# Performance work log

Hardware: AMD Instinct MI355X
Metric: run time of the kernel (lower is better)

Reference implementation:

```python
import jax, jax.numpy as jnp
import numpy as np

DIM = 128
DIM1 = 128
D_MODEL = DIM + DIM1          # 256
D_INNER = 2 * D_MODEL         # expand=2 -> 512
D_STATE = 16
D_CONV = 4
DT_RANK = (D_MODEL + 15) // 16  # ceil(d_model/16) = 16
B, H, W = 4, 64, 64


def layer_norm(x, g, b, eps=1e-5):
    mu = jnp.mean(x, axis=-1, keepdims=True)
    var = jnp.mean((x - mu) ** 2, axis=-1, keepdims=True)
    return (x - mu) * jax.lax.rsqrt(var + eps) * g + b


def setup_inputs() -> dict:
    key = jax.random.key(0)
    ks = jax.random.split(key, 16)
    s = lambda k, shape, scale: (jax.random.normal(k, shape, jnp.float32) * scale)
    inp = {
        "input": jax.random.normal(ks[0], (B, DIM, H, W), jnp.float32),
        "input2": jax.random.normal(ks[1], (B, DIM1, H, W), jnp.float32),
        # MambaB params
        "ln0_g": jnp.ones((D_MODEL,), jnp.float32),
        "ln0_b": jnp.zeros((D_MODEL,), jnp.float32),
        "outp_w": s(ks[2], (D_MODEL, DIM), 1.0 / np.sqrt(D_MODEL)),
        "outp_b": jnp.zeros((DIM,), jnp.float32),
        # Mamba params
        "in_proj_w": s(ks[3], (D_MODEL, 2 * D_INNER), 1.0 / np.sqrt(D_MODEL)),
        "conv_w": s(ks[4], (D_INNER, D_CONV), 1.0 / np.sqrt(D_CONV)),
        "conv_b": jnp.zeros((D_INNER,), jnp.float32),
        "x_proj_w": s(ks[5], (D_INNER, DT_RANK + 2 * D_STATE), 1.0 / np.sqrt(D_INNER)),
        "dt_proj_w": s(ks[6], (DT_RANK, D_INNER), 1.0 / np.sqrt(DT_RANK)),
        "dt_proj_b": s(ks[7], (D_INNER,), 0.1),
        "A_log": jnp.log(jnp.tile(jnp.arange(1.0, D_STATE + 1.0, dtype=jnp.float32), (D_INNER, 1))),
        "D_param": jnp.ones((D_INNER,), jnp.float32),
        "mamba_out_w": s(ks[8], (D_INNER, D_MODEL), 1.0 / np.sqrt(D_INNER)),
    }
    return inp


def mamba(x, in_proj_w, conv_w, conv_b, x_proj_w, dt_proj_w, dt_proj_b, A_log, D_param, mamba_out_w):
    b, L, _ = x.shape
    xz = x @ in_proj_w                       # [b, L, 2*di]
    xs, z = jnp.split(xz, 2, axis=-1)
    # causal depthwise conv over sequence
    xt = xs.transpose(0, 2, 1)               # [b, di, L]
    conv = jax.lax.conv_general_dilated(
        xt, conv_w[:, None, :], window_strides=(1,),
        padding=[(D_CONV - 1, 0)], feature_group_count=D_INNER)
    xs = jax.nn.silu(conv + conv_b[None, :, None]).transpose(0, 2, 1)  # [b, L, di]
    x_dbl = xs @ x_proj_w                    # [b, L, dt_rank + 2*n]
    dt = x_dbl[..., :DT_RANK]
    Bm = x_dbl[..., DT_RANK:DT_RANK + D_STATE]
    Cm = x_dbl[..., DT_RANK + D_STATE:]
    delta = jax.nn.softplus(dt @ dt_proj_w + dt_proj_b)  # [b, L, di]
    A = -jnp.exp(A_log)                      # [di, n]

    def step(h, t):
        d_t, B_t, C_t, x_t = t               # [b,di],[b,n],[b,n],[b,di]
        dA = jnp.exp(d_t[:, :, None] * A)    # [b, di, n]
        h = h * dA + (d_t * x_t)[:, :, None] * B_t[:, None, :]
        y = jnp.einsum('bdn,bn->bd', h, C_t)
        return h, y

    h0 = jnp.zeros((b, D_INNER, D_STATE), x.dtype)
    _, ys = jax.lax.scan(step, h0, (delta.transpose(1, 0, 2), Bm.transpose(1, 0, 2),
                                    Cm.transpose(1, 0, 2), xs.transpose(1, 0, 2)))
    y = ys.transpose(1, 0, 2) + xs * D_param
    y = y * jax.nn.silu(z)
    return y @ mamba_out_w                   # [b, L, d_model]


def reference(input, input2, ln0_g, ln0_b, outp_w, outp_b, in_proj_w, conv_w, conv_b,
              x_proj_w, dt_proj_w, dt_proj_b, A_log, D_param, mamba_out_w):
    b, c, h, w = input.shape
    x = jnp.concatenate((input, input2), axis=1)            # [b, d_model, h, w]
    x = x.reshape(b, D_MODEL, h * w).transpose(0, 2, 1)     # [b, hw, d_model]
    x = layer_norm(x, ln0_g, ln0_b)
    out = mamba(x, in_proj_w, conv_w, conv_b, x_proj_w, dt_proj_w, dt_proj_b,
                A_log, D_param, mamba_out_w)
    out = out @ outp_w + outp_b                             # [b, hw, dim]
    return out.transpose(0, 2, 1).reshape(b, c, h, w)
```

## Files before the change

kernel.cpp:

```cpp
#include <hip/hip_runtime.h>
#include <hip/hip_bf16.h>
#include <math.h>

#define LSEQ 4096
#define NR   16384
#define NB   4
#define CHUNK 32
#define NCH  128

typedef short bf16x8 __attribute__((ext_vector_type(8)));
typedef float f32x4  __attribute__((ext_vector_type(4)));
typedef float f32x2  __attribute__((ext_vector_type(2)));

typedef __attribute__((address_space(1))) const void gvoid_t;
typedef __attribute__((address_space(3))) void svoid_t;

__device__ __forceinline__ void gld_lds16(void* lds, const void* g) {
    __builtin_amdgcn_global_load_lds((gvoid_t*)g, (svoid_t*)lds, 16, 0, 0);
}

__device__ __forceinline__ unsigned short to_bf16(float f) {
    union { float f; unsigned u; } x; x.f = f;
    unsigned r = (x.u + 0x7fff + ((x.u >> 16) & 1)) >> 16;
    return (unsigned short)r;
}
__device__ __forceinline__ float bf2f(unsigned short u) {
    union { unsigned u; float f; } x; x.u = ((unsigned)u) << 16;
    return x.f;
}
__device__ __forceinline__ float softplus_f(float x) {
    return x > 20.f ? x : __logf(1.f + __expf(x));
}
__device__ __forceinline__ float silu_f(float x) {
    return x / (1.f + __expf(-x));
}

__device__ __forceinline__ void pow_chain16_pk(float r, f32x2* a2) {
    float r2 = r * r;
    float r4 = r2 * r2;
    float r8 = r4 * r4;
    f32x2 v01 = { r, r2 };
    a2[0] = v01;
    a2[1] = v01 * r2;
    a2[2] = v01 * r4;
    a2[3] = a2[1] * r4;
    a2[4] = v01 * r8;
    a2[5] = a2[1] * r8;
    a2[6] = a2[2] * r8;
    a2[7] = a2[3] * r8;
}

__device__ __forceinline__ bool pow_ok16(const float* An) {
    bool ok = true;
    #pragma unroll
    for (int n = 1; n < 16; ++n) {
        float ref = (float)(n + 1) * An[0];
        ok = ok && (fabsf(An[n] - ref) <= 1e-4f * fabsf(An[n]) + 1e-30f);
    }
    return ok;
}

__global__ __launch_bounds__(256) void front_kernel(const float* __restrict__ in1,
                                                    const float* __restrict__ in2,
                                                    const float* __restrict__ g,
                                                    const float* __restrict__ beta,
                                                    const float* __restrict__ Wm,
                                                    const float* __restrict__ Wo,
                                                    const float* __restrict__ Wxp,
                                                    const float* __restrict__ A_log,
                                                    const float* __restrict__ W,
                                                    unsigned short* __restrict__ Abf,
                                                    unsigned short* __restrict__ WcT,
                                                    unsigned short* __restrict__ Wxpt,
                                                    float* __restrict__ anegp,
                                                    unsigned short* __restrict__ Wt) {
    __shared__ float tile[256][33];
    int blk = blockIdx.x;
    int tid = threadIdx.x;
    if (blk < 512) {
        __shared__ float s1[8][32], s2[8][32];
        __shared__ float smu[32], srs[32];
        int b  = blk >> 7;
        int t0 = (blk & 127) * 32;
        #pragma unroll
        for (int p = 0; p < 8; ++p) {
            int c = p * 32 + (tid >> 3);
            int toff = (tid & 7) * 4;
            const float* src = (c < 128) ? &in1[((size_t)(b * 128 + c)) * LSEQ + t0 + toff]
                                         : &in2[((size_t)(b * 128 + (c - 128))) * LSEQ + t0 + toff];
            float4 v = *(const float4*)src;
            tile[c][toff] = v.x; tile[c][toff+1] = v.y;
            tile[c][toff+2] = v.z; tile[c][toff+3] = v.w;
        }
        __syncthreads();
        {
            int t = tid & 31, gg = tid >> 5;
            float a1 = 0.f, a2 = 0.f;
            #pragma unroll
            for (int i = 0; i < 32; ++i) {
                float v = tile[gg * 32 + i][t];
                a1 += v; a2 += v * v;
            }
            s1[gg][t] = a1; s2[gg][t] = a2;
        }
        __syncthreads();
        if (tid < 32) {
            float a1 = 0.f, a2 = 0.f;
            #pragma unroll
            for (int gg = 0; gg < 8; ++gg) { a1 += s1[gg][tid]; a2 += s2[gg][tid]; }
            float m = a1 * (1.f / 256.f);
            float var = a2 * (1.f / 256.f) - m * m;
            smu[tid] = m;
            srs[tid] = rsqrtf(var + 1e-5f);
        }
        __syncthreads();
        int c = tid;
        float gc = g[c], bc = beta[c];
        #pragma unroll 4
        for (int t = 0; t < 32; ++t) {
            float v = (tile[c][t] - smu[t]) * srs[t] * gc + bc;
            Abf[((size_t)((b << 12) + t0 + t)) * 256 + c] = to_bf16(v);
        }
    } else if (blk < 768) {
        int gid = (blk - 512) * 256 + tid;
        int row = gid >> 7, col = gid & 127;
        float acc = 0.f;
        #pragma unroll 8
        for (int k = 0; k < 256; ++k) acc += Wm[row * 256 + k] * Wo[k * 128 + col];
        WcT[(size_t)col * 512 + row] = to_bf16(acc);
    } else if (blk < 864) {
        int gid = (blk - 768) * 256 + tid;
        int n = gid >> 9, k = gid & 511;
        Wxpt[gid] = to_bf16(Wxp[(size_t)k * 48 + n]);
    } else if (blk < 896) {
        int gid = (blk - 864) * 256 + tid;
        anegp[gid] = -__expf(A_log[gid]);
    } else {
        float* tf = &tile[0][0];
        int local = blk - 896;
        int k0 = (local & 3) * 64;
        int n0 = (local >> 2) * 64;
        int a = tid & 63, q = tid >> 6;
        #pragma unroll
        for (int i = 0; i < 16; ++i) {
            int k = q * 16 + i;
            tf[k * 65 + a] = W[(size_t)(k0 + k) * 1024 + n0 + a];
        }
        __syncthreads();
        #pragma unroll
        for (int i = 0; i < 16; ++i) {
            int n = q * 16 + i;
            Wt[(size_t)(n0 + n) * 256 + k0 + a] = to_bf16(tf[a * 65 + n]);
        }
    }
}

__global__ __launch_bounds__(256) void gemm1_mfma(const unsigned short* __restrict__ Abf,
                                                  const unsigned short* __restrict__ Wt,
                                                  unsigned short* __restrict__ xh,
                                                  unsigned short* __restrict__ zs) {
    __shared__ __align__(16) short Asl[128][32];
    __shared__ __align__(16) short Bsl[128][32];
    int tid = threadIdx.x;
    int wv = tid >> 6, ln = tid & 63;
    int m0 = blockIdx.x * 128;
    int n0 = blockIdx.y * 128;
    int mw = (wv & 1) * 64, nw = (wv >> 1) * 64;

    f32x4 acc[4][4];
    #pragma unroll
    for (int i = 0; i < 4; ++i)
        #pragma unroll
        for (int j = 0; j < 4; ++j) acc[i][j] = (f32x4)(0.f);

    int srow  = ln >> 2;
    int skoff = (ln & 3) * 8;

    for (int k0 = 0; k0 < 256; k0 += 32) {
        #pragma unroll
        for (int i = 0; i < 2; ++i) {
            int j = wv * 2 + i;
            int row = j * 16 + srow;
            gld_lds16(&Asl[j * 16][0], &Abf[(size_t)(m0 + row) * 256 + k0 + skoff]);
            gld_lds16(&Bsl[j * 16][0], &Wt [(size_t)(n0 + row) * 256 + k0 + skoff]);
        }
        __syncthreads();
        bf16x8 af[4], bff[4];
        int fm = ln & 15, fk = (ln >> 4) * 8;
        #pragma unroll
        for (int i = 0; i < 4; ++i) {
            af[i]  = *(const bf16x8*)&Asl[mw + i * 16 + fm][fk];
            bff[i] = *(const bf16x8*)&Bsl[nw + i * 16 + fm][fk];
        }
        #pragma unroll
        for (int i = 0; i < 4; ++i)
            #pragma unroll
            for (int j = 0; j < 4; ++j)
                acc[i][j] = __builtin_amdgcn_mfma_f32_16x16x32_bf16(af[i], bff[j], acc[i][j], 0, 0, 0);
        __syncthreads();
    }
    int ccol = ln & 15, crow = (ln >> 4) * 4;
    bool zhalf = (n0 >= 512);
    #pragma unroll
    for (int i = 0; i < 4; ++i) {
        #pragma unroll
        for (int j = 0; j < 4; ++j) {
            int n = n0 + nw + j * 16 + ccol;
            #pragma unroll
            for (int r = 0; r < 4; ++r) {
                int m = m0 + mw + i * 16 + crow + r;
                float v = acc[i][j][r];
                if (zhalf) zs[(size_t)m * 512 + (n - 512)] = to_bf16(silu_f(v));
                else       xh[(size_t)m * 512 + n]         = to_bf16(v);
            }
        }
    }
}

__global__ __launch_bounds__(512, 4) void mid_kernel(const unsigned short* __restrict__ xh,
                                                     const float* __restrict__ cw,
                                                     const float* __restrict__ cb,
                                                     const unsigned short* __restrict__ Wxpt,
                                                     const float* __restrict__ Wdt,
                                                     const float* __restrict__ dtb,
                                                     const float* __restrict__ anegp,
                                                     unsigned* __restrict__ dxp,
                                                     float* __restrict__ xdbl,
                                                     float* __restrict__ Sarr,
                                                     float* __restrict__ Harr) {
    __shared__ __align__(16) unsigned short xcs[CHUNK][520];
    __shared__ __align__(16) float xds[CHUNK][48];
    int tid = threadIdx.x;
    int chunk = blockIdx.x & (NCH - 1);
    int b     = blockIdx.x >> 7;
    int d = tid;
    int rbase = (b << 12) + chunk * CHUNK;

    float4 w4 = *(const float4*)&cw[d * 4];
    float cbd = cb[d];
    float An[16];
    #pragma unroll
    for (int n = 0; n < 16; n += 4) {
        float4 v = *(const float4*)&anegp[d * 16 + n];
        An[n] = v.x; An[n+1] = v.y; An[n+2] = v.z; An[n+3] = v.w;
    }
    f32x2 wdt2[8];
    #pragma unroll
    for (int q = 0; q < 8; ++q) {
        wdt2[q].x = Wdt[(2 * q) * 512 + d];
        wdt2[q].y = Wdt[(2 * q + 1) * 512 + d];
    }
    float bd = dtb[d];

    float x0 = 0.f, x1 = 0.f, x2 = 0.f;
    if (chunk > 0) {
        x0 = bf2f(xh[(size_t)(rbase - 3) * 512 + d]);
        x1 = bf2f(xh[(size_t)(rbase - 2) * 512 + d]);
        x2 = bf2f(xh[(size_t)(rbase - 1) * 512 + d]);
    }
    #pragma unroll
    for (int t = 0; t < CHUNK; ++t) {
        float x3 = bf2f(xh[(size_t)(rbase + t) * 512 + d]);
        float a = x0 * w4.x + x1 * w4.y + x2 * w4.z + x3 * w4.w + cbd;
        xcs[t][d] = to_bf16(silu_f(a));
        x0 = x1; x1 = x2; x2 = x3;
    }
    __syncthreads();

    {
        int wv = tid >> 6, ln = tid & 63;
        if (wv < 6) {
            int mt = (wv >= 3) ? 16 : 0;
            int wr = (wv >= 3) ? wv - 3 : wv;
            int nt = wr * 16;
            int fm = ln & 15, fk = (ln >> 4) * 8;
            f32x4 acc = (f32x4)(0.f);
            #pragma unroll 4
            for (int k0 = 0; k0 < 512; k0 += 32) {
                bf16x8 af  = *(const bf16x8*)&xcs[mt + fm][k0 + fk];
                bf16x8 bf_ = *(const bf16x8*)&Wxpt[(size_t)(nt + fm) * 512 + k0 + fk];
                acc = __builtin_amdgcn_mfma_f32_16x16x32_bf16(af, bf_, acc, 0, 0, 0);
            }
            int ccol = ln & 15, crow = (ln >> 4) * 4;
            #pragma unroll
            for (int r = 0; r < 4; ++r)
                xds[mt + crow + r][nt + ccol] = acc[r];
        }
    }
    __syncthreads();

    #pragma unroll
    for (int i = 0; i < 2; ++i) {
        int idx = tid + i * 512;
        int t = idx >> 5, n = idx & 31;
        xdbl[(size_t)(rbase + t) * 32 + n] = xds[t][16 + n];
    }

    bool pm = pow_ok16(An);
    f32x2 h2[8];
    #pragma unroll
    for (int n = 0; n < 8; ++n) h2[n] = (f32x2)(0.f);
    float S = 0.f;
    const float4* xds4 = (const float4*)&xds[0][0];
    if (pm) {
        float An0 = An[0];
        #pragma unroll 4
        for (int t = 0; t < CHUNK; ++t) {
            float4 q0 = xds4[t * 12 + 0], q1 = xds4[t * 12 + 1];
            float4 q2 = xds4[t * 12 + 2], q3 = xds4[t * 12 + 3];
            f32x2 acc2 = { bd, 0.f };
            acc2 = acc2 + (f32x2){q0.x, q0.y} * wdt2[0];
            acc2 = acc2 + (f32x2){q0.z, q0.w} * wdt2[1];
            acc2 = acc2 + (f32x2){q1.x, q1.y} * wdt2[2];
            acc2 = acc2 + (f32x2){q1.z, q1.w} * wdt2[3];
            acc2 = acc2 + (f32x2){q2.x, q2.y} * wdt2[4];
            acc2 = acc2 + (f32x2){q2.z, q2.w} * wdt2[5];
            acc2 = acc2 + (f32x2){q3.x, q3.y} * wdt2[6];
            acc2 = acc2 + (f32x2){q3.z, q3.w} * wdt2[7];
            float a = acc2.x + acc2.y;
            unsigned short dbf = to_bf16(softplus_f(a));
            unsigned short xbf = xcs[t][d];
            float dv = bf2f(dbf), xv = bf2f(xbf);
            dxp[(size_t)(rbase + t) * 512 + d] = (unsigned)dbf | ((unsigned)xbf << 16);
            float dx = dv * xv;
            S += dv;
            f32x2 a2[8];
            pow_chain16_pk(__expf(dv * An0), a2);
            float4 B0 = xds4[t * 12 + 4], B1 = xds4[t * 12 + 5];
            float4 B2 = xds4[t * 12 + 6], B3 = xds4[t * 12 + 7];
            h2[0] = h2[0] * a2[0] + dx * (f32x2){B0.x, B0.y};
            h2[1] = h2[1] * a2[1] + dx * (f32x2){B0.z, B0.w};
            h2[2] = h2[2] * a2[2] + dx * (f32x2){B1.x, B1.y};
            h2[3] = h2[3] * a2[3] + dx * (f32x2){B1.z, B1.w};
            h2[4] = h2[4] * a2[4] + dx * (f32x2){B2.x, B2.y};
            h2[5] = h2[5] * a2[5] + dx * (f32x2){B2.z, B2.w};
            h2[6] = h2[6] * a2[6] + dx * (f32x2){B3.x, B3.y};
            h2[7] = h2[7] * a2[7] + dx * (f32x2){B3.z, B3.w};
        }
    } else {
        #pragma unroll 2
        for (int t = 0; t < CHUNK; ++t) {
            float4 q0 = xds4[t * 12 + 0], q1 = xds4[t * 12 + 1];
            float4 q2 = xds4[t * 12 + 2], q3 = xds4[t * 12 + 3];
            f32x2 acc2 = { bd, 0.f };
            acc2 = acc2 + (f32x2){q0.x, q0.y} * wdt2[0];
            acc2 = acc2 + (f32x2){q0.z, q0.w} * wdt2[1];
            acc2 = acc2 + (f32x2){q1.x, q1.y} * wdt2[2];
            acc2 = acc2 + (f32x2){q1.z, q1.w} * wdt2[3];
            acc2 = acc2 + (f32x2){q2.x, q2.y} * wdt2[4];
            acc2 = acc2 + (f32x2){q2.z, q2.w} * wdt2[5];
            acc2 = acc2 + (f32x2){q3.x, q3.y} * wdt2[6];
            acc2 = acc2 + (f32x2){q3.z, q3.w} * wdt2[7];
            float a = acc2.x + acc2.y;
            unsigned short dbf = to_bf16(softplus_f(a));
            unsigned short xbf = xcs[t][d];
            float dv = bf2f(dbf), xv = bf2f(xbf);
            dxp[(size_t)(rbase + t) * 512 + d] = (unsigned)dbf | ((unsigned)xbf << 16);
            float dx = dv * xv;
            S += dv;
            float4 B0 = xds4[t * 12 + 4], B1 = xds4[t * 12 + 5];
            float4 B2 = xds4[t * 12 + 6], B3 = xds4[t * 12 + 7];
            f32x2 e0 = { __expf(dv * An[0]),  __expf(dv * An[1])  };
            f32x2 e1 = { __expf(dv * An[2]),  __expf(dv * An[3])  };
            f32x2 e2 = { __expf(dv * An[4]),  __expf(dv * An[5])  };
            f32x2 e3 = { __expf(dv * An[6]),  __expf(dv * An[7])  };
            f32x2 e4 = { __expf(dv * An[8]),  __expf(dv * An[9])  };
            f32x2 e5 = { __expf(dv * An[10]), __expf(dv * An[11]) };
            f32x2 e6 = { __expf(dv * An[12]), __expf(dv * An[13]) };
            f32x2 e7 = { __expf(dv * An[14]), __expf(dv * An[15]) };
            h2[0] = h2[0] * e0 + dx * (f32x2){B0.x, B0.y};
            h2[1] = h2[1] * e1 + dx * (f32x2){B0.z, B0.w};
            h2[2] = h2[2] * e2 + dx * (f32x2){B1.x, B1.y};
            h2[3] = h2[3] * e3 + dx * (f32x2){B1.z, B1.w};
            h2[4] = h2[4] * e4 + dx * (f32x2){B2.x, B2.y};
            h2[5] = h2[5] * e5 + dx * (f32x2){B2.z, B2.w};
            h2[6] = h2[6] * e6 + dx * (f32x2){B3.x, B3.y};
            h2[7] = h2[7] * e7 + dx * (f32x2){B3.z, B3.w};
        }
    }
    Sarr[(size_t)chunk * 2048 + b * 512 + d] = S;
    size_t gbase = ((size_t)(b * 512 + d)) * 16;
    size_t coff  = (size_t)chunk * 32768;
    #pragma unroll
    for (int n = 0; n < 4; ++n) {
        *(float4*)&Harr[coff + gbase + n * 4] =
            make_float4(h2[2*n].x, h2[2*n].y, h2[2*n+1].x, h2[2*n+1].y);
    }
}

__global__ __launch_bounds__(128) void scan_pass2(const float* __restrict__ Sarr,
                                                  const float* __restrict__ anegp,
                                                  float* __restrict__ Harr) {
    int gid = blockIdx.x * 128 + threadIdx.x;
    float An = anegp[gid & 8191];
    int sidx = gid >> 4;
    float carry = 0.f;
    #pragma unroll 8
    for (int c = 0; c < NCH; ++c) {
        float S  = Sarr[(size_t)c * 2048 + sidx];
        size_t off = (size_t)c * 32768 + gid;
        float he = Harr[off];
        Harr[off] = carry;
        carry = he + __expf(S * An) * carry;
    }
}

__global__ __launch_bounds__(512, 4) void scan_pass3_out(const unsigned* __restrict__ dxp,
                                                         const unsigned short* __restrict__ zs,
                                                         const float* __restrict__ xdbl,
                                                         const float* __restrict__ anegp,
                                                         const float* __restrict__ Dp,
                                                         const float* __restrict__ Hin,
                                                         const unsigned short* __restrict__ WcT,
                                                         const float* __restrict__ bo,
                                                         float* __restrict__ out) {
    __shared__ __align__(16) unsigned short yl[CHUNK][520];
    __shared__ __align__(16) float4 sB4[CHUNK][4];
    __shared__ __align__(16) float4 sC4[CHUNK][4];
    int tid = threadIdx.x;
    int chunk = blockIdx.x & (NCH - 1);
    int b     = blockIdx.x >> 7;
    int d = tid;
    int rbase = (b << 12) + chunk * CHUNK;
    unsigned pwv[CHUNK];
    #pragma unroll
    for (int t = 0; t < CHUNK; ++t)
        pwv[t] = dxp[(size_t)(rbase + t) * 512 + d];
    {
        float* sBf = (float*)sB4;
        float* sCf = (float*)sC4;
        int t = tid >> 4, n = tid & 15;
        sBf[t * 16 + n] = xdbl[(size_t)(rbase + t) * 32 + n];
        sCf[t * 16 + n] = xdbl[(size_t)(rbase + t) * 32 + 16 + n];
    }
    float An[16];
    #pragma unroll
    for (int n = 0; n < 16; n += 4) {
        float4 v = *(const float4*)&anegp[d * 16 + n];
        An[n] = v.x; An[n+1] = v.y; An[n+2] = v.z; An[n+3] = v.w;
    }
    bool pm = pow_ok16(An);
    float Dv = Dp[d];
    __syncthreads();
    size_t gbase = ((size_t)(b * 512 + d)) * 16;
    size_t coff  = (size_t)chunk * 32768;
    f32x2 h2[8];
    #pragma unroll
    for (int n = 0; n < 4; ++n) {
        float4 v = *(const float4*)&Hin[coff + gbase + n * 4];
        h2[2*n].x = v.x; h2[2*n].y = v.y; h2[2*n+1].x = v.z; h2[2*n+1].y = v.w;
    }
    if (pm) {
        float An0 = An[0];
        #pragma unroll 8
        for (int t = 0; t < CHUNK; ++t) {
            unsigned pw = pwv[t];
            float dv = bf2f((unsigned short)(pw & 0xffffu));
            float xv = bf2f((unsigned short)(pw >> 16));
            float zv = bf2f(zs[(size_t)(rbase + t) * 512 + d]);
            float dx = dv * xv;
            f32x2 a2[8];
            pow_chain16_pk(__expf(dv * An0), a2);
            float4 B0 = sB4[t][0], B1 = sB4[t][1], B2 = sB4[t][2], B3 = sB4[t][3];
            float4 C0 = sC4[t][0], C1 = sC4[t][1], C2 = sC4[t][2], C3 = sC4[t][3];
            f32x2 y2 = (f32x2)(0.f);
            h2[0] = h2[0] * a2[0] + dx * (f32x2){B0.x, B0.y};  y2 = y2 + h2[0] * (f32x2){C0.x, C0.y};
            h2[1] = h2[1] * a2[1] + dx * (f32x2){B0.z, B0.w};  y2 = y2 + h2[1] * (f32x2){C0.z, C0.w};
            h2[2] = h2[2] * a2[2] + dx * (f32x2){B1.x, B1.y};  y2 = y2 + h2[2] * (f32x2){C1.x, C1.y};
            h2[3] = h2[3] * a2[3] + dx * (f32x2){B1.z, B1.w};  y2 = y2 + h2[3] * (f32x2){C1.z, C1.w};
            h2[4] = h2[4] * a2[4] + dx * (f32x2){B2.x, B2.y};  y2 = y2 + h2[4] * (f32x2){C2.x, C2.y};
            h2[5] = h2[5] * a2[5] + dx * (f32x2){B2.z, B2.w};  y2 = y2 + h2[5] * (f32x2){C2.z, C2.w};
            h2[6] = h2[6] * a2[6] + dx * (f32x2){B3.x, B3.y};  y2 = y2 + h2[6] * (f32x2){C3.x, C3.y};
            h2[7] = h2[7] * a2[7] + dx * (f32x2){B3.z, B3.w};  y2 = y2 + h2[7] * (f32x2){C3.z, C3.w};
            float y = y2.x + y2.y + xv * Dv;
            y *= zv;
            yl[t][d] = to_bf16(y);
        }
    } else {
        #pragma unroll 4
        for (int t = 0; t < CHUNK; ++t) {
            unsigned pw = pwv[t];
            float dv = bf2f((unsigned short)(pw & 0xffffu));
            float xv = bf2f((unsigned short)(pw >> 16));
            float zv = bf2f(zs[(size_t)(rbase + t) * 512 + d]);
            float dx = dv * xv;
            float4 B0 = sB4[t][0], B1 = sB4[t][1], B2 = sB4[t][2], B3 = sB4[t][3];
            float4 C0 = sC4[t][0], C1 = sC4[t][1], C2 = sC4[t][2], C3 = sC4[t][3];
            f32x2 e0 = { __expf(dv * An[0]),  __expf(dv * An[1])  };
            f32x2 e1 = { __expf(dv * An[2]),  __expf(dv * An[3])  };
            f32x2 e2 = { __expf(dv * An[4]),  __expf(dv * An[5])  };
            f32x2 e3 = { __expf(dv * An[6]),  __expf(dv * An[7])  };
            f32x2 e4 = { __expf(dv * An[8]),  __expf(dv * An[9])  };
            f32x2 e5 = { __expf(dv * An[10]), __expf(dv * An[11]) };
            f32x2 e6 = { __expf(dv * An[12]), __expf(dv * An[13]) };
            f32x2 e7 = { __expf(dv * An[14]), __expf(dv * An[15]) };
            f32x2 y2 = (f32x2)(0.f);
            h2[0] = h2[0] * e0 + dx * (f32x2){B0.x, B0.y};  y2 = y2 + h2[0] * (f32x2){C0.x, C0.y};
            h2[1] = h2[1] * e1 + dx * (f32x2){B0.z, B0.w};  y2 = y2 + h2[1] * (f32x2){C0.z, C0.w};
            h2[2] = h2[2] * e2 + dx * (f32x2){B1.x, B1.y};  y2 = y2 + h2[2] * (f32x2){C1.x, C1.y};
            h2[3] = h2[3] * e3 + dx * (f32x2){B1.z, B1.w};  y2 = y2 + h2[3] * (f32x2){C1.z, C1.w};
            h2[4] = h2[4] * e4 + dx * (f32x2){B2.x, B2.y};  y2 = y2 + h2[4] * (f32x2){C2.x, C2.y};
            h2[5] = h2[5] * e5 + dx * (f32x2){B2.z, B2.w};  y2 = y2 + h2[5] * (f32x2){C2.z, C2.w};
            h2[6] = h2[6] * e6 + dx * (f32x2){B3.x, B3.y};  y2 = y2 + h2[6] * (f32x2){C3.x, C3.y};
            h2[7] = h2[7] * e7 + dx * (f32x2){B3.z, B3.w};  y2 = y2 + h2[7] * (f32x2){C3.z, C3.w};
            float y = y2.x + y2.y + xv * Dv;
            y *= zv;
            yl[t][d] = to_bf16(y);
        }
    }
    __syncthreads();

    {
        int wv = tid >> 6, ln = tid & 63;
        int fm = ln & 15, fk = (ln >> 4) * 8;
        f32x4 acc0 = (f32x4)(0.f), acc1 = (f32x4)(0.f);
        const unsigned short* wrow = &WcT[(size_t)(wv * 16 + fm) * 512];
        #pragma unroll 4
        for (int k0 = 0; k0 < 512; k0 += 32) {
            bf16x8 af = *(const bf16x8*)&wrow[k0 + fk];
            bf16x8 b0 = *(const bf16x8*)&yl[fm][k0 + fk];
            bf16x8 b1 = *(const bf16x8*)&yl[16 + fm][k0 + fk];
            acc0 = __builtin_amdgcn_mfma_f32_16x16x32_bf16(af, b0, acc0, 0, 0, 0);
            acc1 = __builtin_amdgcn_mfma_f32_16x16x32_bf16(af, b1, acc1, 0, 0, 0);
        }
        int ccol = ln & 15, crow = (ln >> 4) * 4;
        #pragma unroll
        for (int r = 0; r < 4; ++r) {
            int c = wv * 16 + crow + r;
            float bias = bo[c];
            size_t obase = ((size_t)(b * 128 + c)) * LSEQ + chunk * CHUNK;
            out[obase + ccol]      = acc0[r] + bias;
            out[obase + 16 + ccol] = acc1[r] + bias;
        }
    }
}

extern "C" void kernel_launch(void* const* d_in, const int* in_sizes, int n_in,
                              void* d_out, int out_size, void* d_ws, size_t ws_size,
                              hipStream_t stream) {
    (void)in_sizes; (void)n_in; (void)out_size; (void)ws_size;
    const float* input    = (const float*)d_in[0];
    const float* input2   = (const float*)d_in[1];
    const float* ln_g     = (const float*)d_in[2];
    const float* ln_b     = (const float*)d_in[3];
    const float* outp_w   = (const float*)d_in[4];
    const float* outp_b   = (const float*)d_in[5];
    const float* in_proj  = (const float*)d_in[6];
    const float* conv_w   = (const float*)d_in[7];
    const float* conv_b   = (const float*)d_in[8];
    const float* x_proj   = (const float*)d_in[9];
    const float* dt_w     = (const float*)d_in[10];
    const float* dt_b     = (const float*)d_in[11];
    const float* A_log    = (const float*)d_in[12];
    const float* D_param  = (const float*)d_in[13];
    const float* mout_w   = (const float*)d_in[14];
    float* out = (float*)d_out;

    char* ws = (char*)d_ws;
    unsigned short* xh    = (unsigned short*)ws;                    ws += (size_t)NR * 512 * 2;
    unsigned short* zsbuf = (unsigned short*)ws;                    ws += (size_t)NR * 512 * 2;
    unsigned*       dxp   = (unsigned*)ws;                          ws += (size_t)NR * 512 * 4;
    unsigned short* Abf   = (unsigned short*)ws;                    ws += (size_t)NR * 256 * 2;
    unsigned short* Wt    = (unsigned short*)ws;                    ws += (size_t)1024 * 256 * 2;
    unsigned short* WcT   = (unsigned short*)ws;                    ws += (size_t)128 * 512 * 2;
    unsigned short* Wxpt  = (unsigned short*)ws;                    ws += (size_t)48 * 512 * 2;
    float* anegp = (float*)ws;                                      ws += (size_t)512 * 16 * 4;
    float* xdbl = (float*)ws;                                       ws += (size_t)NR * 32 * 4;
    float* Sarr = (float*)ws;                                       ws += (size_t)NCH * 2048 * 4;
    float* Harr = (float*)ws;                                       ws += (size_t)NCH * 32768 * 4;

    front_kernel<<<960, 256, 0, stream>>>(input, input2, ln_g, ln_b, mout_w, outp_w,
                                          x_proj, A_log, in_proj,
                                          Abf, WcT, Wxpt, anegp, Wt);
    gemm1_mfma<<<dim3(128, 8), 256, 0, stream>>>(Abf, Wt, xh, zsbuf);
    mid_kernel<<<NB * NCH, 512, 0, stream>>>(xh, conv_w, conv_b, Wxpt, dt_w, dt_b,
                                             anegp, dxp, xdbl, Sarr, Harr);
    scan_pass2<<<256, 128, 0, stream>>>(Sarr, anegp, Harr);
    scan_pass3_out<<<NB * NCH, 512, 0, stream>>>(dxp, zsbuf, xdbl, anegp, D_param,
                                                 Harr, WcT, outp_b, out);
}
```

Before: 197.5 us.

## Compute x and z halves in one gemm1 block and swizzle block order

Each gemm1 block now computes both the x-part and the z-part output tiles for the same rows, so every A tile loaded into LDS is reused for two B tiles. The grid drops from 1024 blocks to 512 and uses a 1D index remapped so neighbouring blocks share A rows, for better L2 locality. This halves A traffic but doubles the accumulator registers (32 f32x4 per thread), which may lower occupancy or cause spills.

New measurement: 201.9 us. +2.2%, slower.

```diff
diff --git a/kernel.cpp b/kernel.cpp
--- a/kernel.cpp
+++ b/kernel.cpp
@@ -160,18 +160,23 @@
                                                   unsigned short* __restrict__ xh,
                                                   unsigned short* __restrict__ zs) {
     __shared__ __align__(16) short Asl[128][32];
-    __shared__ __align__(16) short Bsl[128][32];
+    __shared__ __align__(16) short Bs1[128][32];
+    __shared__ __align__(16) short Bs2[128][32];
     int tid = threadIdx.x;
     int wv = tid >> 6, ln = tid & 63;
-    int m0 = blockIdx.x * 128;
-    int n0 = blockIdx.y * 128;
+    int j = blockIdx.x;
+    int x = j & 7, s = j >> 3;
+    int mt = x + 8 * (s >> 2);
+    int np = s & 3;
+    int m0 = mt * 128;
+    int n0 = np * 128;
     int mw = (wv & 1) * 64, nw = (wv >> 1) * 64;
 
-    f32x4 acc[4][4];
+    f32x4 acc1[4][4], acc2[4][4];
     #pragma unroll
     for (int i = 0; i < 4; ++i)
         #pragma unroll
-        for (int j = 0; j < 4; ++j) acc[i][j] = (f32x4)(0.f);
+        for (int jj = 0; jj < 4; ++jj) { acc1[i][jj] = (f32x4)(0.f); acc2[i][jj] = (f32x4)(0.f); }
 
     int srow  = ln >> 2;
     int skoff = (ln & 3) * 8;
@@ -179,39 +184,41 @@
     for (int k0 = 0; k0 < 256; k0 += 32) {
         #pragma unroll
         for (int i = 0; i < 2; ++i) {
-            int j = wv * 2 + i;
-            int row = j * 16 + srow;
-            gld_lds16(&Asl[j * 16][0], &Abf[(size_t)(m0 + row) * 256 + k0 + skoff]);
-            gld_lds16(&Bsl[j * 16][0], &Wt [(size_t)(n0 + row) * 256 + k0 + skoff]);
+            int jr = wv * 2 + i;
+            int row = jr * 16 + srow;
+            gld_lds16(&Asl[jr * 16][0], &Abf[(size_t)(m0 + row) * 256 + k0 + skoff]);
+            gld_lds16(&Bs1[jr * 16][0], &Wt [(size_t)(n0 + row) * 256 + k0 + skoff]);
+            gld_lds16(&Bs2[jr * 16][0], &Wt [(size_t)(n0 + 512 + row) * 256 + k0 + skoff]);
         }
         __syncthreads();
-        bf16x8 af[4], bff[4];
+        bf16x8 af[4], b1f[4], b2f[4];
         int fm = ln & 15, fk = (ln >> 4) * 8;
         #pragma unroll
         for (int i = 0; i < 4; ++i) {
             af[i]  = *(const bf16x8*)&Asl[mw + i * 16 + fm][fk];
-            bff[i] = *(const bf16x8*)&Bsl[nw + i * 16 + fm][fk];
+            b1f[i] = *(const bf16x8*)&Bs1[nw + i * 16 + fm][fk];
+            b2f[i] = *(const bf16x8*)&Bs2[nw + i * 16 + fm][fk];
         }
         #pragma unroll
         for (int i = 0; i < 4; ++i)
             #pragma unroll
-            for (int j = 0; j < 4; ++j)
-                acc[i][j] = __builtin_amdgcn_mfma_f32_16x16x32_bf16(af[i], bff[j], acc[i][j], 0, 0, 0);
+            for (int jj = 0; jj < 4; ++jj) {
+                acc1[i][jj] = __builtin_amdgcn_mfma_f32_16x16x32_bf16(af[i], b1f[jj], acc1[i][jj], 0, 0, 0);
+                acc2[i][jj] = __builtin_amdgcn_mfma_f32_16x16x32_bf16(af[i], b2f[jj], acc2[i][jj], 0, 0, 0);
+            }
         __syncthreads();
     }
     int ccol = ln & 15, crow = (ln >> 4) * 4;
-    bool zhalf = (n0 >= 512);
     #pragma unroll
     for (int i = 0; i < 4; ++i) {
         #pragma unroll
-        for (int j = 0; j < 4; ++j) {
-            int n = n0 + nw + j * 16 + ccol;
+        for (int jj = 0; jj < 4; ++jj) {
+            int n = n0 + nw + jj * 16 + ccol;
             #pragma unroll
             for (int r = 0; r < 4; ++r) {
                 int m = m0 + mw + i * 16 + crow + r;
-                float v = acc[i][j][r];
-                if (zhalf) zs[(size_t)m * 512 + (n - 512)] = to_bf16(silu_f(v));
-                else       xh[(size_t)m * 512 + n]         = to_bf16(v);
+                xh[(size_t)m * 512 + n] = to_bf16(acc1[i][jj][r]);
+                zs[(size_t)m * 512 + n] = to_bf16(silu_f(acc2[i][jj][r]));
             }
         }
     }
@@ -572,7 +579,7 @@
     front_kernel<<<960, 256, 0, stream>>>(input, input2, ln_g, ln_b, mout_w, outp_w,
                                           x_proj, A_log, in_proj,
                                           Abf, WcT, Wxpt, anegp, Wt);
-    gemm1_mfma<<<dim3(128, 8), 256, 0, stream>>>(Abf, Wt, xh, zsbuf);
+    gemm1_mfma<<<512, 256, 0, stream>>>(Abf, Wt, xh, zsbuf);
     mid_kernel<<<NB * NCH, 512, 0, stream>>>(xh, conv_w, conv_b, Wxpt, dt_w, dt_b,
                                              anegp, dxp, xdbl, Sarr, Harr);
     scan_pass2<<<256, 128, 0, stream>>>(Sarr, anegp, Harr);
```
